# Performance work log

Measured on AMD Instinct MI355X. Metric: run time of the kernel, lower is better.

The kernel has to match this reference:

```python
import jax, jax.numpy as jnp
import numpy as np

NUM_NODES = 100000
NUM_EDGES = 1600000
INPUT_DIM = 128
NUM_LAYERS = 3
EPS = 1e-12


def setup_inputs() -> dict:
    key = jax.random.key(0)
    k1, k2, k3, k4, k5 = jax.random.split(key, 5)
    emb = jax.random.normal(k1, (NUM_NODES, INPUT_DIM), dtype=jnp.float32)
    edge_index = jax.random.randint(k2, (2, NUM_EDGES), 0, NUM_NODES, dtype=jnp.int64)
    senders = jax.random.randint(k3, (16384,), 0, NUM_NODES, dtype=jnp.int64)
    receivers = jax.random.randint(k4, (16384,), 0, NUM_NODES, dtype=jnp.int64)
    mlp_dim = INPUT_DIM * (NUM_LAYERS + 1)  # concat aggregation -> 512
    W = jax.random.normal(k5, (mlp_dim, mlp_dim), dtype=jnp.float32) * 0.02
    b = jnp.zeros((mlp_dim,), dtype=jnp.float32)
    return {"emb": emb, "edge_index": edge_index, "senders": senders,
            "receivers": receivers, "W": W, "b": b}


def _l2_normalize(x):
    # matches F.normalize(x, p=2, dim=-1) with eps=1e-12
    n = jnp.linalg.norm(x, axis=-1, keepdims=True)
    return x / jnp.maximum(n, EPS)


def reference(emb, edge_index, senders, receivers, W, b):
    src, dst = edge_index[0], edge_index[1]
    # LightGCN-style symmetric degree normalization: 1/sqrt(d_src * d_dst)
    ones = jnp.ones((src.shape[0],), dtype=emb.dtype)
    deg = jax.ops.segment_sum(ones, dst, num_segments=NUM_NODES)
    deg = jnp.maximum(deg, 1.0)
    dinv = jax.lax.rsqrt(deg)
    norm = dinv[src] * dinv[dst]  # [E]

    x = emb
    z = [_l2_normalize(x)]
    for _ in range(NUM_LAYERS):
        msgs = x[src] * norm[:, None]                      # [E, D] gather + scale
        x = jax.ops.segment_sum(msgs, dst, num_segments=NUM_NODES)  # scatter-add
        z.append(_l2_normalize(x))
    x = jnp.concatenate(z, axis=-1)        # [N, D*(L+1)]
    x = x @ W.T + b                        # post_mlp
    return (x[senders], x[receivers])
```

## Files before the change

### kernel.cpp

```cpp
#include <hip/hip_runtime.h>

#define NN 100000
#define NE 1600000
#define DD 128
#define MD 512
#define SEL 16384
#define MROWS 32768
#define NBKT 196
#define TILE 4096
#define SEGCAP 16384

typedef __attribute__((ext_vector_type(8))) short bf16x8;
typedef __attribute__((ext_vector_type(4))) float f32x4;

__device__ __forceinline__ unsigned short f2bf(float f) {
  unsigned u = __float_as_uint(f);
  u += 0x7fff + ((u >> 16) & 1);
  return (unsigned short)(u >> 16);
}
__device__ __forceinline__ float bflo(unsigned v) { return __uint_as_float(v << 16); }
__device__ __forceinline__ float bfhi(unsigned v) { return __uint_as_float(v & 0xffff0000u); }

__global__ __launch_bounds__(256) void k_binA(const int* __restrict__ src,
                                              const int* __restrict__ dst,
                                              int* __restrict__ gcursor,
                                              unsigned* __restrict__ ebuf) {
  __shared__ int hist[NBKT];
  __shared__ int base[NBKT];
  __shared__ int cnt2[NBKT];
  const int tid = threadIdx.x;
  const long e0 = (long)blockIdx.x * TILE;
  for (int i = tid; i < NBKT; i += 256) { hist[i] = 0; cnt2[i] = 0; }
  __syncthreads();
  unsigned pk[16]; int bk[16];
  #pragma unroll
  for (int k = 0; k < 16; ++k) {
    const long e = e0 + k * 256 + tid;
    bk[k] = -1;
    if (e < NE) {
      const int d = dst[e], s = src[e];
      bk[k] = d >> 9;
      pk[k] = ((unsigned)s << 9) | (unsigned)(d & 511);
      atomicAdd(&hist[bk[k]], 1);
    }
  }
  __syncthreads();
  for (int i = tid; i < NBKT; i += 256)
    base[i] = i * SEGCAP + atomicAdd(&gcursor[i], hist[i]);
  __syncthreads();
  #pragma unroll
  for (int k = 0; k < 16; ++k) {
    if (bk[k] >= 0) {
      const int lp = atomicAdd(&cnt2[bk[k]], 1);
      ebuf[base[bk[k]] + lp] = pk[k];
    }
  }
}

__global__ __launch_bounds__(256) void k_degB(const unsigned* __restrict__ ebuf,
                                              const int* __restrict__ bcnt,
                                              int* __restrict__ deg,
                                              float* __restrict__ dinv,
                                              int* __restrict__ excl,
                                              int* __restrict__ btot,
                                              unsigned short* __restrict__ x0,
                                              unsigned short* __restrict__ x1,
                                              unsigned short* __restrict__ x2) {
  __shared__ int ld[512];
  __shared__ int ps[256];
  const int b = blockIdx.x;
  const int n0 = b << 9;
  const int nn = min(512, NN - n0);
  const int tid = threadIdx.x;
  for (int i = tid; i < 512; i += 256) ld[i] = 0;
  __syncthreads();
  const int s0 = b * SEGCAP;
  const int c = bcnt[b];
  for (int i = tid; i < c; i += 256) atomicAdd(&ld[ebuf[s0 + i] & 511], 1);
  __syncthreads();
  const int d0 = (tid * 2 < nn) ? ld[tid * 2] : 0;
  const int d1 = (tid * 2 + 1 < nn) ? ld[tid * 2 + 1] : 0;
  const int p0 = (d0 + 7) & ~7, p1 = (d1 + 7) & ~7;
  ps[tid] = p0 + p1;
  __syncthreads();
  for (int o = 1; o < 256; o <<= 1) {
    int t2 = (tid >= o) ? ps[tid - o] : 0;
    __syncthreads();
    ps[tid] += t2;
    __syncthreads();
  }
  const int exbase = ps[tid] - (p0 + p1);
  if (tid * 2 < nn) {
    deg[n0 + tid * 2] = d0;
    dinv[n0 + tid * 2] = rsqrtf(fmaxf((float)d0, 1.f));
    excl[n0 + tid * 2] = exbase;
  }
  if (tid * 2 + 1 < nn) {
    deg[n0 + tid * 2 + 1] = d1;
    dinv[n0 + tid * 2 + 1] = rsqrtf(fmaxf((float)d1, 1.f));
    excl[n0 + tid * 2 + 1] = exbase + p0;
  }
  if (tid == 255) btot[b] = ps[255];
  if (b == 0 && tid < 64) {
    ((unsigned*)(x0 + (size_t)NN * DD))[tid] = 0u;
    ((unsigned*)(x1 + (size_t)NN * DD))[tid] = 0u;
    ((unsigned*)(x2 + (size_t)NN * DD))[tid] = 0u;
  }
}

__global__ __launch_bounds__(256) void k_binB(const unsigned* __restrict__ ebuf,
                                              const int* __restrict__ bcnt,
                                              const int* __restrict__ btot,
                                              const int* __restrict__ excl,
                                              int* __restrict__ rowstart,
                                              int* __restrict__ csr) {
  __shared__ int seg[SEGCAP];
  __shared__ int rs[512];
  __shared__ int cnt[512];
  __shared__ int sm[256];
  const int b = blockIdx.x;
  const int n0 = b << 9;
  const int nn = min(512, NN - n0);
  const int tid = threadIdx.x;
  int v = (tid < NBKT) ? btot[tid] : 0;
  sm[tid] = v;
  __syncthreads();
  for (int o = 1; o < 256; o <<= 1) {
    int t2 = (tid >= o) ? sm[tid - o] : 0;
    __syncthreads();
    sm[tid] += t2;
    __syncthreads();
  }
  const int seg0 = b ? sm[b - 1] : 0;
  const int seglen = btot[b];
  for (int i = tid; i < nn; i += 256) {
    const int ex = excl[n0 + i];
    rs[i] = ex;
    cnt[i] = 0;
    rowstart[n0 + i] = seg0 + ex;
  }
  for (int i = tid; i < seglen; i += 256) seg[i] = NN;
  __syncthreads();
  const int s0 = b * SEGCAP;
  const int c = bcnt[b];
  for (int i = tid; i < c; i += 256) {
    const unsigned e = ebuf[s0 + i];
    const int dl = e & 511;
    const int pos = rs[dl] + atomicAdd(&cnt[dl], 1);
    seg[pos] = (int)(e >> 9);
  }
  __syncthreads();
  for (int i = tid; i < seglen; i += 256) csr[seg0 + i] = seg[i];
}

__global__ void k_mark(const int* __restrict__ sl, const int* __restrict__ rl,
                       int* __restrict__ mark) {
  int i = blockIdx.x * blockDim.x + threadIdx.x;
  if (i < SEL) mark[sl[i]] = 1;
  else if (i < 2 * SEL) mark[rl[i - SEL]] = 1;
}

__global__ void k_compact(const int* __restrict__ mark, int* __restrict__ list,
                          int* __restrict__ cnt, int* __restrict__ uidx) {
  int n = blockIdx.x * blockDim.x + threadIdx.x;
  if (n < NN && mark[n]) {
    int p = atomicAdd(cnt, 1);
    list[p] = n;
    uidx[n] = p;
  }
}

template<int WX>
__global__ __launch_bounds__(256) void k_aggs(const int* __restrict__ rowstart,
                                              const int* __restrict__ deg,
                                              const int* __restrict__ csr,
                                              const float* __restrict__ dinv,
                                              const unsigned short* __restrict__ xin,
                                              unsigned short* __restrict__ xout,
                                              const int* __restrict__ list,
                                              const int* __restrict__ lcnt) {
  const int lane = threadIdx.x & 63;
  const int hi = lane >> 5, l5 = lane & 31;
  const int bid = blockIdx.x;
  const int xcd = bid & 7;
  const int h = xcd >> 2;
  const int g = (bid >> 3) * 4 + (xcd & 3);
  const int wvh = g * 4 + (threadIdx.x >> 6);
  const int stride = gridDim.x * 2;
  const int xoff = h * 64;
  const int total = WX ? NN : *lcnt;
  for (int p = wvh; 2 * p < total; p += stride) {
    const int idx = 2 * p + hi;
    const bool act = idx < total;
    const int n = act ? (WX ? idx : list[idx]) : 0;
    const int start = rowstart[n];
    const int cntp = act ? ((deg[n] + 7) & ~7) : 0;
    float ax[8], ay[8];
    #pragma unroll
    for (int u = 0; u < 8; ++u) { ax[u] = 0.f; ay[u] = 0.f; }
    for (int j = 0; j < cntp; j += 8) {
      const int4 e0 = *(const int4*)(csr + start + j);
      const int4 e1 = *(const int4*)(csr + start + j + 4);
      unsigned v[8];
      v[0] = ((const unsigned*)(xin + (size_t)e0.x * DD + xoff))[l5];
      v[1] = ((const unsigned*)(xin + (size_t)e0.y * DD + xoff))[l5];
      v[2] = ((const unsigned*)(xin + (size_t)e0.z * DD + xoff))[l5];
      v[3] = ((const unsigned*)(xin + (size_t)e0.w * DD + xoff))[l5];
      v[4] = ((const unsigned*)(xin + (size_t)e1.x * DD + xoff))[l5];
      v[5] = ((const unsigned*)(xin + (size_t)e1.y * DD + xoff))[l5];
      v[6] = ((const unsigned*)(xin + (size_t)e1.z * DD + xoff))[l5];
      v[7] = ((const unsigned*)(xin + (size_t)e1.w * DD + xoff))[l5];
      #pragma unroll
      for (int u = 0; u < 8; ++u) { ax[u] += bflo(v[u]); ay[u] += bfhi(v[u]); }
    }
    if (act) {
      const float s = dinv[n] * dinv[n];
      const float rx = (((ax[0] + ax[1]) + (ax[2] + ax[3])) + ((ax[4] + ax[5]) + (ax[6] + ax[7]))) * s;
      const float ry = (((ay[0] + ay[1]) + (ay[2] + ay[3])) + ((ay[4] + ay[5]) + (ay[6] + ay[7]))) * s;
      const size_t orow = WX ? (size_t)n : (size_t)idx;
      ((unsigned*)(xout + orow * DD + xoff))[l5] =
          ((unsigned)f2bf(ry) << 16) | f2bf(rx);
    }
  }
}

__global__ __launch_bounds__(256) void k_zall(const int* __restrict__ list,
                                              const int* __restrict__ lcnt,
                                              const unsigned short* __restrict__ x0,
                                              const unsigned short* __restrict__ x1,
                                              const unsigned short* __restrict__ x2,
                                              const unsigned short* __restrict__ u3c,
                                              unsigned short* __restrict__ zbuf) {
  const int lane = threadIdx.x & 63;
  const int wv = (blockIdx.x * blockDim.x + threadIdx.x) >> 6;
  const int nw = (gridDim.x * blockDim.x) >> 6;
  const int cl = *lcnt;
  for (int r = wv; r < cl; r += nw) {
    const int node = list[r];
    unsigned v[4];
    v[0] = ((const unsigned*)(x0 + (size_t)node * DD))[lane];
    v[1] = ((const unsigned*)(x1 + (size_t)node * DD))[lane];
    v[2] = ((const unsigned*)(x2 + (size_t)node * DD))[lane];
    v[3] = ((const unsigned*)(u3c + (size_t)r * DD))[lane];
    #pragma unroll
    for (int q = 0; q < 4; ++q) {
      const float a = bflo(v[q]), b = bfhi(v[q]);
      float ss = fmaf(a, a, b * b);
      #pragma unroll
      for (int m = 32; m >= 1; m >>= 1) ss += __shfl_xor(ss, m);
      const float sc = 1.0f / fmaxf(sqrtf(ss), 1e-12f);
      *(unsigned*)(zbuf + (size_t)r * MD + q * DD + lane * 2) =
          ((unsigned)f2bf(b * sc) << 16) | f2bf(a * sc);
    }
  }
}

__global__ __launch_bounds__(256) void k_conv_emb2(const float* __restrict__ emb,
                                                   const float* __restrict__ dinv,
                                                   unsigned short* __restrict__ x0,
                                                   const float* __restrict__ W,
                                                   unsigned short* __restrict__ Wbf) {
  if (blockIdx.x >= NN / 4) {
    const int i = (blockIdx.x - NN / 4) * 256 + threadIdx.x;
    if (i < MD * MD / 4) {
      float4 v = ((const float4*)W)[i];
      ushort4 o;
      o.x = f2bf(v.x); o.y = f2bf(v.y); o.z = f2bf(v.z); o.w = f2bf(v.w);
      ((ushort4*)Wbf)[i] = o;
    }
    return;
  }
  const int lane = threadIdx.x & 63;
  const int n = blockIdx.x * 4 + (threadIdx.x >> 6);
  const float2 v = ((const float2*)(emb + (size_t)n * DD))[lane];
  const float d = dinv[n];
  *(unsigned*)(x0 + (size_t)n * DD + lane * 2) =
      ((unsigned)f2bf(v.y * d) << 16) | f2bf(v.x * d);
}

__global__ __launch_bounds__(256) void k_gemm(const unsigned short* __restrict__ zbuf,
                                              const int* __restrict__ sl,
                                              const int* __restrict__ rl,
                                              const int* __restrict__ uidx,
                                              const unsigned short* __restrict__ B,
                                              const float* __restrict__ bias,
                                              float* __restrict__ out) {
  __shared__ __align__(16) char smraw[20480];
  unsigned short (*As)[40] = (unsigned short(*)[40])smraw;
  unsigned short (*Bs)[40] = (unsigned short(*)[40])(smraw + 10240);
  float (*et)[132] = (float(*)[132])smraw;
  const int t = threadIdx.x;
  const int bid = blockIdx.x;
  const int xcd = bid & 7;
  const int j = bid >> 3;
  const int mt = xcd * 32 + (j >> 2);
  const int nt = j & 3;
  const int i0 = mt * 128, j0 = nt * 128;
  const int lane = t & 63, wid = t >> 6;
  const int wr = wid >> 1, wc = wid & 1;
  const int fr = lane & 15, kg = lane >> 4;
  const int srow = t >> 2, seg = t & 3;
  const int r0 = i0 + srow, r1 = r0 + 64;
  const int nd0 = (r0 < SEL) ? sl[r0] : rl[r0 - SEL];
  const int nd1 = (r1 < SEL) ? sl[r1] : rl[r1 - SEL];
  const unsigned short* pa0 = zbuf + (size_t)uidx[nd0] * MD + seg * 8;
  const unsigned short* pa1 = zbuf + (size_t)uidx[nd1] * MD + seg * 8;
  const unsigned short* pb0 = B + (size_t)(j0 + srow) * MD + seg * 8;
  const unsigned short* pb1 = B + (size_t)(j0 + srow + 64) * MD + seg * 8;
  f32x4 acc[4][4] = {};
  for (int k0 = 0; k0 < MD; k0 += 32) {
    *(float4*)(&As[srow][seg * 8]) = *(const float4*)(pa0 + k0);
    *(float4*)(&As[srow + 64][seg * 8]) = *(const float4*)(pa1 + k0);
    *(float4*)(&Bs[srow][seg * 8]) = *(const float4*)(pb0 + k0);
    *(float4*)(&Bs[srow + 64][seg * 8]) = *(const float4*)(pb1 + k0);
    __syncthreads();
    bf16x8 af[4], bfr[4];
    #pragma unroll
    for (int m = 0; m < 4; ++m)
      af[m] = *(const bf16x8*)(&As[wr * 64 + m * 16 + fr][kg * 8]);
    #pragma unroll
    for (int n = 0; n < 4; ++n)
      bfr[n] = *(const bf16x8*)(&Bs[wc * 64 + n * 16 + fr][kg * 8]);
    #pragma unroll
    for (int m = 0; m < 4; ++m)
      #pragma unroll
      for (int n = 0; n < 4; ++n)
        acc[m][n] = __builtin_amdgcn_mfma_f32_16x16x32_bf16(af[m], bfr[n], acc[m][n], 0, 0, 0);
    __syncthreads();
  }
  #pragma unroll
  for (int m = 0; m < 4; ++m) {
    __syncthreads();
    #pragma unroll
    for (int n = 0; n < 4; ++n)
      #pragma unroll
      for (int r = 0; r < 4; ++r)
        et[wr * 16 + kg * 4 + r][wc * 64 + n * 16 + fr] = acc[m][n][r];
    __syncthreads();
    #pragma unroll
    for (int w = 0; w < 4; ++w) {
      const int idx = w * 256 + t;
      const int lrow = idx >> 5, lc4 = idx & 31;
      const int grow = i0 + (lrow >> 4) * 64 + m * 16 + (lrow & 15);
      const int gcol = j0 + lc4 * 4;
      const float4 bv = *(const float4*)(bias + gcol);
      float4 o;
      o.x = et[lrow][lc4 * 4 + 0] + bv.x;
      o.y = et[lrow][lc4 * 4 + 1] + bv.y;
      o.z = et[lrow][lc4 * 4 + 2] + bv.z;
      o.w = et[lrow][lc4 * 4 + 3] + bv.w;
      *(float4*)(out + (size_t)grow * MD + gcol) = o;
    }
  }
}

extern "C" void kernel_launch(void* const* d_in, const int* in_sizes, int n_in,
                              void* d_out, int out_size, void* d_ws, size_t ws_size,
                              hipStream_t stream) {
  const float* emb = (const float*)d_in[0];
  const int* ei = (const int*)d_in[1];
  const int* esrc = ei;
  const int* edst = ei + NE;
  const int* send = (const int*)d_in[2];
  const int* recv = (const int*)d_in[3];
  const float* W = (const float*)d_in[4];
  const float* bias = (const float*)d_in[5];
  float* out = (float*)d_out;

  char* ws = (char*)d_ws;
  size_t off = 0;
  auto take = [&](size_t b) {
    char* p = ws + off;
    off = (off + b + 1023) & ~(size_t)1023;
    return p;
  };
  const size_t CSRN = (size_t)NE + 8 * (size_t)NN;
  int* zblk = (int*)take((size_t)(NBKT + 1 + NN) * 4);
  int* gcursor = zblk;
  int* lcnt = zblk + NBKT;
  int* mark = zblk + NBKT + 1;
  int* uidx = (int*)take((size_t)NN * 4);
  float* dinv = (float*)take((size_t)NN * 4);
  int* degI = (int*)take((size_t)NN * 4);
  int* rowstart = (int*)take((size_t)NN * 4);
  int* excl = (int*)take((size_t)NN * 4);
  int* btot = (int*)take(NBKT * 4);
  int* list = (int*)take((size_t)MROWS * 4);
  unsigned* ebuf = (unsigned*)take((size_t)NBKT * SEGCAP * 4);
  int* csr = (int*)take(CSRN * 4);
  unsigned short* x0 = (unsigned short*)take((size_t)(NN + 1) * DD * 2);
  unsigned short* x1 = (unsigned short*)take((size_t)(NN + 1) * DD * 2);
  unsigned short* x2 = (unsigned short*)take((size_t)(NN + 1) * DD * 2);
  unsigned short* u3c = (unsigned short*)take((size_t)MROWS * DD * 2);
  unsigned short* zbuf = (unsigned short*)take((size_t)MROWS * MD * 2);
  unsigned short* Wbf = (unsigned short*)take((size_t)MD * MD * 2);
  (void)ws_size; (void)in_sizes; (void)n_in; (void)out_size;

  hipMemsetAsync(zblk, 0, (size_t)(NBKT + 1 + NN) * 4, stream);
  hipMemsetAsync(uidx, 0xFF, (size_t)NN * 4, stream);

  k_binA<<<(NE + TILE - 1) / TILE, 256, 0, stream>>>(esrc, edst, gcursor, ebuf);
  k_degB<<<NBKT, 256, 0, stream>>>(ebuf, gcursor, degI, dinv, excl, btot, x0, x1, x2);
  k_binB<<<NBKT, 256, 0, stream>>>(ebuf, gcursor, btot, excl, rowstart, csr);

  k_mark<<<(2 * SEL + 255) / 256, 256, 0, stream>>>(send, recv, mark);
  k_compact<<<(NN + 255) / 256, 256, 0, stream>>>(mark, list, lcnt, uidx);
  k_conv_emb2<<<NN / 4 + MD * MD / 4 / 256, 256, 0, stream>>>(emb, dinv, x0, W, Wbf);

  k_aggs<1><<<2048, 256, 0, stream>>>(rowstart, degI, csr, dinv, x0, x1, list, lcnt);
  k_aggs<1><<<2048, 256, 0, stream>>>(rowstart, degI, csr, dinv, x1, x2, list, lcnt);
  k_aggs<0><<<1024, 256, 0, stream>>>(rowstart, degI, csr, dinv, x2, u3c, list, lcnt);

  k_zall<<<1024, 256, 0, stream>>>(list, lcnt, x0, x1, x2, u3c, zbuf);
  k_gemm<<<(MROWS / 128) * (MD / 128), 256, 0, stream>>>(zbuf, send, recv, uidx,
                                                         Wbf, bias, out);
}
```

Measured before the change: 287.9 us.

## Fuse setup kernels and merge final-layer aggregation with normalization

The mark pass is folded into the edge-binning kernel as extra blocks, and the compaction pass is folded into the degree kernel. The separate uidx memset is dropped, since only marked nodes are ever read. The third-layer aggregation for the selected rows is fused with the L2-normalize/concat kernel, which removes the u3c intermediate buffer and one launch. The grid size of the first two aggregation launches is also doubled. The aim is to cut launch overhead and intermediate memory traffic, at the cost of heterogeneous blocks within the fused kernels and a different per-wave work split for layer 3.

```diff
diff --git a/kernel.cpp b/kernel.cpp
--- a/kernel.cpp
+++ b/kernel.cpp
@@ -9,6 +9,9 @@
 #define NBKT 196
 #define TILE 4096
 #define SEGCAP 16384
+#define NBINA ((NE + TILE - 1) / TILE)
+#define NMARK ((2 * SEL + 255) / 256)
+#define NCOMP ((NN + 255) / 256)
 
 typedef __attribute__((ext_vector_type(8))) short bf16x8;
 typedef __attribute__((ext_vector_type(4))) float f32x4;
@@ -21,10 +24,19 @@
 __device__ __forceinline__ float bflo(unsigned v) { return __uint_as_float(v << 16); }
 __device__ __forceinline__ float bfhi(unsigned v) { return __uint_as_float(v & 0xffff0000u); }
 
-__global__ __launch_bounds__(256) void k_binA(const int* __restrict__ src,
-                                              const int* __restrict__ dst,
-                                              int* __restrict__ gcursor,
-                                              unsigned* __restrict__ ebuf) {
+__global__ __launch_bounds__(256) void k_binA_mark(const int* __restrict__ src,
+                                                   const int* __restrict__ dst,
+                                                   int* __restrict__ gcursor,
+                                                   unsigned* __restrict__ ebuf,
+                                                   const int* __restrict__ sl,
+                                                   const int* __restrict__ rl,
+                                                   int* __restrict__ mark) {
+  if (blockIdx.x >= NBINA) {
+    const int i = (blockIdx.x - NBINA) * 256 + threadIdx.x;
+    if (i < SEL) mark[sl[i]] = 1;
+    else if (i < 2 * SEL) mark[rl[i - SEL]] = 1;
+    return;
+  }
   __shared__ int hist[NBKT];
   __shared__ int base[NBKT];
   __shared__ int cnt2[NBKT];
@@ -57,15 +69,28 @@
   }
 }
 
-__global__ __launch_bounds__(256) void k_degB(const unsigned* __restrict__ ebuf,
-                                              const int* __restrict__ bcnt,
-                                              int* __restrict__ deg,
-                                              float* __restrict__ dinv,
-                                              int* __restrict__ excl,
-                                              int* __restrict__ btot,
-                                              unsigned short* __restrict__ x0,
-                                              unsigned short* __restrict__ x1,
-                                              unsigned short* __restrict__ x2) {
+__global__ __launch_bounds__(256) void k_degB_compact(const unsigned* __restrict__ ebuf,
+                                                      const int* __restrict__ bcnt,
+                                                      int* __restrict__ deg,
+                                                      float* __restrict__ dinv,
+                                                      int* __restrict__ excl,
+                                                      int* __restrict__ btot,
+                                                      unsigned short* __restrict__ x0,
+                                                      unsigned short* __restrict__ x1,
+                                                      unsigned short* __restrict__ x2,
+                                                      const int* __restrict__ mark,
+                                                      int* __restrict__ list,
+                                                      int* __restrict__ lcnt,
+                                                      int* __restrict__ uidx) {
+  if (blockIdx.x >= NBKT) {
+    const int n = (blockIdx.x - NBKT) * 256 + threadIdx.x;
+    if (n < NN && mark[n]) {
+      const int p = atomicAdd(lcnt, 1);
+      list[p] = n;
+      uidx[n] = p;
+    }
+    return;
+  }
   __shared__ int ld[512];
   __shared__ int ps[256];
   const int b = blockIdx.x;
@@ -153,32 +178,12 @@
   for (int i = tid; i < seglen; i += 256) csr[seg0 + i] = seg[i];
 }
 
-__global__ void k_mark(const int* __restrict__ sl, const int* __restrict__ rl,
-                       int* __restrict__ mark) {
-  int i = blockIdx.x * blockDim.x + threadIdx.x;
-  if (i < SEL) mark[sl[i]] = 1;
-  else if (i < 2 * SEL) mark[rl[i - SEL]] = 1;
-}
-
-__global__ void k_compact(const int* __restrict__ mark, int* __restrict__ list,
-                          int* __restrict__ cnt, int* __restrict__ uidx) {
-  int n = blockIdx.x * blockDim.x + threadIdx.x;
-  if (n < NN && mark[n]) {
-    int p = atomicAdd(cnt, 1);
-    list[p] = n;
-    uidx[n] = p;
-  }
-}
-
-template<int WX>
 __global__ __launch_bounds__(256) void k_aggs(const int* __restrict__ rowstart,
                                               const int* __restrict__ deg,
                                               const int* __restrict__ csr,
                                               const float* __restrict__ dinv,
                                               const unsigned short* __restrict__ xin,
-                                              unsigned short* __restrict__ xout,
-                                              const int* __restrict__ list,
-                                              const int* __restrict__ lcnt) {
+                                              unsigned short* __restrict__ xout) {
   const int lane = threadIdx.x & 63;
   const int hi = lane >> 5, l5 = lane & 31;
   const int bid = blockIdx.x;
@@ -188,11 +193,10 @@
   const int wvh = g * 4 + (threadIdx.x >> 6);
   const int stride = gridDim.x * 2;
   const int xoff = h * 64;
-  const int total = WX ? NN : *lcnt;
-  for (int p = wvh; 2 * p < total; p += stride) {
+  for (int p = wvh; 2 * p < NN; p += stride) {
     const int idx = 2 * p + hi;
-    const bool act = idx < total;
-    const int n = act ? (WX ? idx : list[idx]) : 0;
+    const bool act = idx < NN;
+    const int n = act ? idx : 0;
     const int start = rowstart[n];
     const int cntp = act ? ((deg[n] + 7) & ~7) : 0;
     float ax[8], ay[8];
@@ -217,34 +221,66 @@
       const float s = dinv[n] * dinv[n];
       const float rx = (((ax[0] + ax[1]) + (ax[2] + ax[3])) + ((ax[4] + ax[5]) + (ax[6] + ax[7]))) * s;
       const float ry = (((ay[0] + ay[1]) + (ay[2] + ay[3])) + ((ay[4] + ay[5]) + (ay[6] + ay[7]))) * s;
-      const size_t orow = WX ? (size_t)n : (size_t)idx;
-      ((unsigned*)(xout + orow * DD + xoff))[l5] =
+      ((unsigned*)(xout + (size_t)n * DD + xoff))[l5] =
           ((unsigned)f2bf(ry) << 16) | f2bf(rx);
     }
   }
 }
 
-__global__ __launch_bounds__(256) void k_zall(const int* __restrict__ list,
-                                              const int* __restrict__ lcnt,
-                                              const unsigned short* __restrict__ x0,
-                                              const unsigned short* __restrict__ x1,
-                                              const unsigned short* __restrict__ x2,
-                                              const unsigned short* __restrict__ u3c,
-                                              unsigned short* __restrict__ zbuf) {
+__global__ __launch_bounds__(256) void k_agg3z(const int* __restrict__ rowstart,
+                                               const int* __restrict__ deg,
+                                               const int* __restrict__ csr,
+                                               const float* __restrict__ dinv,
+                                               const unsigned short* __restrict__ x0,
+                                               const unsigned short* __restrict__ x1,
+                                               const unsigned short* __restrict__ x2,
+                                               unsigned short* __restrict__ zbuf,
+                                               const int* __restrict__ list,
+                                               const int* __restrict__ lcnt) {
   const int lane = threadIdx.x & 63;
   const int wv = (blockIdx.x * blockDim.x + threadIdx.x) >> 6;
   const int nw = (gridDim.x * blockDim.x) >> 6;
   const int cl = *lcnt;
   for (int r = wv; r < cl; r += nw) {
-    const int node = list[r];
-    unsigned v[4];
-    v[0] = ((const unsigned*)(x0 + (size_t)node * DD))[lane];
-    v[1] = ((const unsigned*)(x1 + (size_t)node * DD))[lane];
-    v[2] = ((const unsigned*)(x2 + (size_t)node * DD))[lane];
-    v[3] = ((const unsigned*)(u3c + (size_t)r * DD))[lane];
-    #pragma unroll
-    for (int q = 0; q < 4; ++q) {
-      const float a = bflo(v[q]), b = bfhi(v[q]);
+    const int n = list[r];
+    const int start = rowstart[n];
+    const int cntp = (deg[n] + 7) & ~7;
+    float ax[8], ay[8];
+    #pragma unroll
+    for (int u = 0; u < 8; ++u) { ax[u] = 0.f; ay[u] = 0.f; }
+    for (int j = 0; j < cntp; j += 8) {
+      const int4 e0 = *(const int4*)(csr + start + j);
+      const int4 e1 = *(const int4*)(csr + start + j + 4);
+      unsigned v[8];
+      v[0] = ((const unsigned*)(x2 + (size_t)e0.x * DD))[lane];
+      v[1] = ((const unsigned*)(x2 + (size_t)e0.y * DD))[lane];
+      v[2] = ((const unsigned*)(x2 + (size_t)e0.z * DD))[lane];
+      v[3] = ((const unsigned*)(x2 + (size_t)e0.w * DD))[lane];
+      v[4] = ((const unsigned*)(x2 + (size_t)e1.x * DD))[lane];
+      v[5] = ((const unsigned*)(x2 + (size_t)e1.y * DD))[lane];
+      v[6] = ((const unsigned*)(x2 + (size_t)e1.z * DD))[lane];
+      v[7] = ((const unsigned*)(x2 + (size_t)e1.w * DD))[lane];
+      #pragma unroll
+      for (int u = 0; u < 8; ++u) { ax[u] += bflo(v[u]); ay[u] += bfhi(v[u]); }
+    }
+    const float s = dinv[n] * dinv[n];
+    const float rx = (((ax[0] + ax[1]) + (ax[2] + ax[3])) + ((ax[4] + ax[5]) + (ax[6] + ax[7]))) * s;
+    const float ry = (((ay[0] + ay[1]) + (ay[2] + ay[3])) + ((ay[4] + ay[5]) + (ay[6] + ay[7]))) * s;
+    {
+      float ss = fmaf(rx, rx, ry * ry);
+      #pragma unroll
+      for (int m = 32; m >= 1; m >>= 1) ss += __shfl_xor(ss, m);
+      const float sc = 1.0f / fmaxf(sqrtf(ss), 1e-12f);
+      *(unsigned*)(zbuf + (size_t)r * MD + 384 + lane * 2) =
+          ((unsigned)f2bf(ry * sc) << 16) | f2bf(rx * sc);
+    }
+    unsigned v0 = ((const unsigned*)(x0 + (size_t)n * DD))[lane];
+    unsigned v1 = ((const unsigned*)(x1 + (size_t)n * DD))[lane];
+    unsigned v2 = ((const unsigned*)(x2 + (size_t)n * DD))[lane];
+    unsigned vv[3] = {v0, v1, v2};
+    #pragma unroll
+    for (int q = 0; q < 3; ++q) {
+      const float a = bflo(vv[q]), b = bfhi(vv[q]);
       float ss = fmaf(a, a, b * b);
       #pragma unroll
       for (int m = 32; m >= 1; m >>= 1) ss += __shfl_xor(ss, m);
@@ -391,27 +427,25 @@
   unsigned short* x0 = (unsigned short*)take((size_t)(NN + 1) * DD * 2);
   unsigned short* x1 = (unsigned short*)take((size_t)(NN + 1) * DD * 2);
   unsigned short* x2 = (unsigned short*)take((size_t)(NN + 1) * DD * 2);
-  unsigned short* u3c = (unsigned short*)take((size_t)MROWS * DD * 2);
   unsigned short* zbuf = (unsigned short*)take((size_t)MROWS * MD * 2);
   unsigned short* Wbf = (unsigned short*)take((size_t)MD * MD * 2);
   (void)ws_size; (void)in_sizes; (void)n_in; (void)out_size;
 
   hipMemsetAsync(zblk, 0, (size_t)(NBKT + 1 + NN) * 4, stream);
-  hipMemsetAsync(uidx, 0xFF, (size_t)NN * 4, stream);
-
-  k_binA<<<(NE + TILE - 1) / TILE, 256, 0, stream>>>(esrc, edst, gcursor, ebuf);
-  k_degB<<<NBKT, 256, 0, stream>>>(ebuf, gcursor, degI, dinv, excl, btot, x0, x1, x2);
+
+  k_binA_mark<<<NBINA + NMARK, 256, 0, stream>>>(esrc, edst, gcursor, ebuf,
+                                                 send, recv, mark);
+  k_degB_compact<<<NBKT + NCOMP, 256, 0, stream>>>(ebuf, gcursor, degI, dinv, excl,
+                                                   btot, x0, x1, x2, mark, list,
+                                                   lcnt, uidx);
   k_binB<<<NBKT, 256, 0, stream>>>(ebuf, gcursor, btot, excl, rowstart, csr);
-
-  k_mark<<<(2 * SEL + 255) / 256, 256, 0, stream>>>(send, recv, mark);
-  k_compact<<<(NN + 255) / 256, 256, 0, stream>>>(mark, list, lcnt, uidx);
   k_conv_emb2<<<NN / 4 + MD * MD / 4 / 256, 256, 0, stream>>>(emb, dinv, x0, W, Wbf);
 
-  k_aggs<1><<<2048, 256, 0, stream>>>(rowstart, degI, csr, dinv, x0, x1, list, lcnt);
-  k_aggs<1><<<2048, 256, 0, stream>>>(rowstart, degI, csr, dinv, x1, x2, list, lcnt);
-  k_aggs<0><<<1024, 256, 0, stream>>>(rowstart, degI, csr, dinv, x2, u3c, list, lcnt);
-
-  k_zall<<<1024, 256, 0, stream>>>(list, lcnt, x0, x1, x2, u3c, zbuf);
+  k_aggs<<<4096, 256, 0, stream>>>(rowstart, degI, csr, dinv, x0, x1);
+  k_aggs<<<4096, 256, 0, stream>>>(rowstart, degI, csr, dinv, x1, x2);
+  k_agg3z<<<2048, 256, 0, stream>>>(rowstart, degI, csr, dinv, x0, x1, x2,
+                                    zbuf, list, lcnt);
+
   k_gemm<<<(MROWS / 128) * (MD / 128), 256, 0, stream>>>(zbuf, send, recv, uidx,
                                                          Wbf, bias, out);
 }
```

Result: faster. 263.3 us (-8.5%).
